# Kernel optimization log

Hardware: AMD Instinct MI355X
Metric: run time of the kernel (lower is better)

## Reference

```python
import jax, jax.numpy as jnp
import numpy as np

B, T, C = 2, 2048, 1024
N_HEAD = 16
HEAD_DIM = C // N_HEAD


def setup_inputs() -> dict:
    key = jax.random.key(0)
    k1, k2, k3, k4, k5 = jax.random.split(key, 5)
    s = 1.0 / np.sqrt(C)
    return {
        "x": jax.random.normal(k1, (B, T, C), dtype=jnp.float32),
        "w_attn": jax.random.normal(k2, (C, 3 * C), dtype=jnp.float32) * s,
        "b_attn": jax.random.normal(k3, (3 * C,), dtype=jnp.float32) * 0.02,
        "w_proj": jax.random.normal(k4, (C, C), dtype=jnp.float32) * s,
        "b_proj": jax.random.normal(k5, (C,), dtype=jnp.float32) * 0.02,
    }


def reference(x, w_attn, b_attn, w_proj, b_proj):
    Bx, Tx, Cx = x.shape
    qkv = x @ w_attn + b_attn  # [B, T, 3C]
    q, k, v = jnp.split(qkv, 3, axis=2)
    # [B, H, T, D]
    q = q.reshape(Bx, Tx, N_HEAD, HEAD_DIM).transpose(0, 2, 1, 3)
    k = k.reshape(Bx, Tx, N_HEAD, HEAD_DIM).transpose(0, 2, 1, 3)
    v = v.reshape(Bx, Tx, N_HEAD, HEAD_DIM).transpose(0, 2, 1, 3)
    scale = 1.0 / jnp.sqrt(jnp.asarray(HEAD_DIM, dtype=x.dtype))
    att = jnp.einsum("bhqd,bhkd->bhqk", q, k) * scale  # [B,H,T,T]
    causal = jnp.tril(jnp.ones((Tx, Tx), dtype=bool))
    att = jnp.where(causal[None, None, :, :], att, -jnp.inf)
    att = jax.nn.softmax(att, axis=-1)
    y = jnp.einsum("bhqk,bhkd->bhqd", att, v)  # [B,H,T,D]
    y = y.transpose(0, 2, 1, 3).reshape(Bx, Tx, Cx)
    return y @ w_proj + b_proj
```

## Files before the change

### kernel.cpp

```cpp
#include <hip/hip_runtime.h>
#include <hip/hip_bf16.h>
#include <stdint.h>

#define TT 2048
#define CC 1024
#define NH 16
#define HD 64
#define BT 4096

typedef float f32x4 __attribute__((ext_vector_type(4)));
typedef __bf16 bf16x8 __attribute__((ext_vector_type(8)));
typedef __bf16 bf16x4 __attribute__((ext_vector_type(4)));
typedef short sh4 __attribute__((ext_vector_type(4)));

#define MFMA(a, b, c) __builtin_amdgcn_mfma_f32_16x16x32_bf16((a), (b), (c), 0, 0, 0)
#define MFMA16(a, b, c) __builtin_amdgcn_mfma_f32_16x16x16bf16_1k((a), (b), (c), 0, 0, 0)

__device__ __forceinline__ void gload16(const void* g, void* l) {
    __builtin_amdgcn_global_load_lds(
        (const __attribute__((address_space(1))) void*)g,
        (__attribute__((address_space(3))) void*)l,
        16, 0, 0);
}

__global__ __launch_bounds__(256) void conv_f32_bf16(
    const float* __restrict__ in, __bf16* __restrict__ out, int n4) {
    int i = blockIdx.x * blockDim.x + threadIdx.x;
    int stride = gridDim.x * blockDim.x;
    for (; i < n4; i += stride) {
        float4 v = reinterpret_cast<const float4*>(in)[i];
        bf16x4 o;
        o.x = (__bf16)v.x; o.y = (__bf16)v.y; o.z = (__bf16)v.z; o.w = (__bf16)v.w;
        reinterpret_cast<bf16x4*>(out)[i] = o;
    }
}

__global__ __launch_bounds__(256) void transpose2_f32_bf16(
    const float* __restrict__ wa, __bf16* __restrict__ oa,
    const float* __restrict__ wp, __bf16* __restrict__ op) {
    __shared__ float tile[32][33];
    int bx = blockIdx.x;
    const float* in;
    __bf16* out;
    int C;
    if (bx < 96) { in = wa; out = oa; C = 3072; }
    else         { in = wp; out = op; C = 1024; bx -= 96; }
    int c0 = bx * 32, r0 = blockIdx.y * 32;
    int tx = threadIdx.x & 31, ty = (threadIdx.x >> 5) & 7;
#pragma unroll
    for (int j = 0; j < 32; j += 8)
        tile[ty + j][tx] = in[(size_t)(r0 + ty + j) * C + c0 + tx];
    __syncthreads();
#pragma unroll
    for (int j = 0; j < 32; j += 8)
        out[(size_t)(c0 + ty + j) * 1024 + r0 + tx] = (__bf16)tile[tx][ty + j];
}

template <int MODE>
__global__ __launch_bounds__(256) void gemm128(
    const __bf16* __restrict__ A, const __bf16* __restrict__ Bt,
    const float* __restrict__ bias,
    __bf16* __restrict__ oq, __bf16* __restrict__ ok, __bf16* __restrict__ ov,
    float* __restrict__ of, int M, int N, int K) {
    __shared__ __align__(16) __bf16 As[128 * 64];
    __shared__ __align__(16) __bf16 Bs[128 * 64];
    const int tid = threadIdx.x;
    const int w = tid >> 6, lane = tid & 63;
    const int l15 = lane & 15, lg = lane >> 4;
    const int m0 = blockIdx.y * 128, n0 = blockIdx.x * 128;
    const int wr = w >> 1, wc = w & 1;

    const f32x4 zero4 = {0.f, 0.f, 0.f, 0.f};
    f32x4 acc[4][4];
#pragma unroll
    for (int m = 0; m < 4; ++m)
#pragma unroll
        for (int n = 0; n < 4; ++n) acc[m][n] = zero4;

    const char* Ab = (const char*)A;
    const char* Bb = (const char*)Bt;
    const size_t rowbytes = (size_t)K * 2;

    for (int kt = 0; kt < K; kt += 64) {
#pragma unroll
        for (int j = 0; j < 4; ++j) {
            int base = (w * 4 + j) * 1024;
            int d0 = base + lane * 16;
            int row = d0 >> 7;
            int colb = d0 & 127;
            int scolb = colb ^ ((row & 7) << 4);
            gload16(Ab + (size_t)(m0 + row) * rowbytes + (size_t)kt * 2 + scolb,
                    (char*)As + base);
            gload16(Bb + (size_t)(n0 + row) * rowbytes + (size_t)kt * 2 + scolb,
                    (char*)Bs + base);
        }
        __syncthreads();
#pragma unroll
        for (int kk = 0; kk < 2; ++kk) {
            bf16x8 af[4], bfr[4];
#pragma unroll
            for (int m = 0; m < 4; ++m) {
                int row = wr * 64 + m * 16 + l15;
                int colb = kk * 64 + lg * 16;
                af[m] = *(const bf16x8*)((const char*)As + row * 128 +
                                         (colb ^ ((row & 7) << 4)));
            }
#pragma unroll
            for (int n = 0; n < 4; ++n) {
                int row = wc * 64 + n * 16 + l15;
                int colb = kk * 64 + lg * 16;
                bfr[n] = *(const bf16x8*)((const char*)Bs + row * 128 +
                                          (colb ^ ((row & 7) << 4)));
            }
#pragma unroll
            for (int m = 0; m < 4; ++m)
#pragma unroll
                for (int n = 0; n < 4; ++n)
                    acc[m][n] = MFMA(af[m], bfr[n], acc[m][n]);
        }
        __syncthreads();
    }

#pragma unroll
    for (int n = 0; n < 4; ++n) {
        int col = n0 + wc * 64 + n * 16 + l15;
        float bs = bias[col];
        if constexpr (MODE == 0) {
            int sec = col >> 10;
            int cc = col & 1023;
            int h = cc >> 6, d = cc & 63;
            if (sec == 2) {
#pragma unroll
                for (int m = 0; m < 4; ++m) {
                    int rowb = m0 + wr * 64 + m * 16 + lg * 4;
                    int bb = rowb >> 11, t = rowb & 2047;
                    bf16x4 pk;
#pragma unroll
                    for (int r = 0; r < 4; ++r) pk[r] = (__bf16)(acc[m][n][r] + bs);
                    *(bf16x4*)&ov[((size_t)(bb * NH + h) * HD + d) * TT + t] = pk;
                }
            } else {
                __bf16* dst = (sec == 0) ? oq : ok;
                float mult = (sec == 0) ? 0.125f * 1.44269504088896340736f : 1.0f;
#pragma unroll
                for (int m = 0; m < 4; ++m) {
                    int rowb = m0 + wr * 64 + m * 16 + lg * 4;
#pragma unroll
                    for (int r = 0; r < 4; ++r) {
                        int row = rowb + r;
                        int bb = row >> 11, t = row & 2047;
                        float val = (acc[m][n][r] + bs) * mult;
                        dst[((size_t)(bb * NH + h) * TT + t) * HD + d] = (__bf16)val;
                    }
                }
            }
        } else {
#pragma unroll
            for (int m = 0; m < 4; ++m) {
                int rowb = m0 + wr * 64 + m * 16 + lg * 4;
#pragma unroll
                for (int r = 0; r < 4; ++r) {
                    int row = rowb + r;
                    of[(size_t)row * N + col] = acc[m][n][r] + bs;
                }
            }
        }
    }
}

__global__ __launch_bounds__(256) void attn_kernel(
    const __bf16* __restrict__ q, const __bf16* __restrict__ k,
    const __bf16* __restrict__ vt, __bf16* __restrict__ y) {
    __shared__ __align__(16) __bf16 Kb[2][64 * 64];
    __shared__ __align__(16) __bf16 Vb[2][64 * 64];

    const int n = blockIdx.x;
    const int qt = 31 - (n >> 5);
    const int bh = ((n & 7) << 2) | ((n >> 3) & 3);
    const int tid = threadIdx.x, w = tid >> 6, lane = tid & 63;
    const int l15 = lane & 15, lg = lane >> 4;
    const char* kh = (const char*)(k + (size_t)bh * TT * HD);
    const char* vh = (const char*)(vt + (size_t)bh * HD * TT);
    const __bf16* qh = q + (size_t)bh * TT * HD;
    const int qbw = qt * 64 + w * 16;

    const f32x4 zero4 = {0.f, 0.f, 0.f, 0.f};
    float mrun = -1e30f, lrun = 0.f;
    f32x4 oacc[4];
    bf16x8 qf[2];
#pragma unroll
    for (int f = 0; f < 4; ++f) oacc[f] = zero4;
#pragma unroll
    for (int kk = 0; kk < 2; ++kk)
        qf[kk] = *(const bf16x8*)&qh[(size_t)(qbw + l15) * HD + kk * 32 + lg * 8];

    auto stage = [&](int kvb, int buf) {
#pragma unroll
        for (int j = 0; j < 2; ++j) {
            int d0 = ((w * 2 + j) * 64 + lane) * 16;
            int row = d0 >> 7, colb = d0 & 127;
            int scolb = colb ^ ((row & 7) << 4);
            gload16(kh + (size_t)(kvb + row) * 128 + scolb, (char*)Kb[buf] + d0);
            gload16(vh + (size_t)row * (TT * 2) + (size_t)kvb * 2 + scolb,
                    (char*)Vb[buf] + d0);
        }
    };

    stage(0, 0);
    __syncthreads();

    for (int g = 0; g <= qt; ++g) {
        const int cur = g & 1;
        if (g < qt) stage((g + 1) * 64, cur ^ 1);
        const int kb = g * 64;

        f32x4 s[4];
#pragma unroll
        for (int kf = 0; kf < 4; ++kf) s[kf] = zero4;
        __builtin_amdgcn_s_setprio(1);
#pragma unroll
        for (int kf = 0; kf < 4; ++kf) {
            int krow = kf * 16 + l15;
            const char* kr = (const char*)Kb[cur] + krow * 128;
            bf16x8 k0 = *(const bf16x8*)(kr + ((lg * 16) ^ ((krow & 7) << 4)));
            bf16x8 k1 = *(const bf16x8*)(kr + ((64 + lg * 16) ^ ((krow & 7) << 4)));
            s[kf] = MFMA(k0, qf[0], s[kf]);
            s[kf] = MFMA(k1, qf[1], s[kf]);
        }
        __builtin_amdgcn_s_setprio(0);
        if (g == qt) {
            const int qq = qbw + l15;
#pragma unroll
            for (int kf = 0; kf < 4; ++kf)
#pragma unroll
                for (int r = 0; r < 4; ++r) {
                    int kk_ = kb + kf * 16 + lg * 4 + r;
                    if (kk_ > qq) s[kf][r] = -1e30f;
                }
        }
        f32x4 m01, m23;
#pragma unroll
        for (int r = 0; r < 4; ++r) {
            m01[r] = fmaxf(s[0][r], s[1][r]);
            m23[r] = fmaxf(s[2][r], s[3][r]);
        }
        float m_ = fmaxf(fmaxf(fmaxf(m01[0], m01[1]), fmaxf(m01[2], m01[3])),
                         fmaxf(fmaxf(m23[0], m23[1]), fmaxf(m23[2], m23[3])));
        m_ = fmaxf(m_, __shfl_xor(m_, 16));
        m_ = fmaxf(m_, __shfl_xor(m_, 32));
        if (!__all(m_ <= mrun)) {
            float mn = fmaxf(mrun, m_);
            float fac = exp2f(mrun - mn);
            mrun = mn;
            lrun *= fac;
#pragma unroll
            for (int f = 0; f < 4; ++f)
#pragma unroll
                for (int r = 0; r < 4; ++r) oacc[f][r] *= fac;
        }
        float ss = 0.f;
        sh4 pb[4];
#pragma unroll
        for (int kf = 0; kf < 4; ++kf) {
            bf16x4 pk;
#pragma unroll
            for (int r = 0; r < 4; ++r) {
                float p = exp2f(s[kf][r] - mrun);
                pk[r] = (__bf16)p;
                ss += p;
            }
            pb[kf] = __builtin_bit_cast(sh4, pk);
        }
        lrun += ss;
        __builtin_amdgcn_s_setprio(1);
#pragma unroll
        for (int kf = 0; kf < 4; ++kf) {
#pragma unroll
            for (int f = 0; f < 4; ++f) {
                int vrow = f * 16 + l15;
                bf16x4 va = *(const bf16x4*)((const char*)Vb[cur] + vrow * 128 +
                                ((kf * 32 + lg * 8) ^ ((vrow & 7) << 4)));
                oacc[f] = MFMA16(__builtin_bit_cast(sh4, va), pb[kf], oacc[f]);
            }
        }
        __builtin_amdgcn_s_setprio(0);
        __syncthreads();
    }

    lrun += __shfl_xor(lrun, 16);
    lrun += __shfl_xor(lrun, 32);
    const int b = bh >> 4, h = bh & 15;
    float inv = 1.0f / lrun;
#pragma unroll
    for (int f = 0; f < 4; ++f) {
        bf16x4 pk;
#pragma unroll
        for (int r = 0; r < 4; ++r) pk[r] = (__bf16)(oacc[f][r] * inv);
        *(bf16x4*)&y[(size_t)(b * TT + qbw + l15) * CC + h * 64 + f * 16 +
                     lg * 4] = pk;
    }
}

extern "C" void kernel_launch(void* const* d_in, const int* in_sizes, int n_in,
                              void* d_out, int out_size, void* d_ws, size_t ws_size,
                              hipStream_t stream) {
    const float* x      = (const float*)d_in[0];
    const float* w_attn = (const float*)d_in[1];
    const float* b_attn = (const float*)d_in[2];
    const float* w_proj = (const float*)d_in[3];
    const float* b_proj = (const float*)d_in[4];
    float* out = (float*)d_out;

    char* ws = (char*)d_ws;
    size_t off = 0;
    auto alloc = [&](size_t bytes) {
        char* p = ws + off;
        off += (bytes + 255) & ~(size_t)255;
        return p;
    };
    __bf16* xb   = (__bf16*)alloc((size_t)BT * CC * 2);
    __bf16* watb = (__bf16*)alloc((size_t)3 * CC * CC * 2);
    __bf16* wptb = (__bf16*)alloc((size_t)CC * CC * 2);
    __bf16* qb   = (__bf16*)alloc((size_t)BT * CC * 2);
    __bf16* kbuf = (__bf16*)alloc((size_t)BT * CC * 2);
    __bf16* vtb  = (__bf16*)alloc((size_t)BT * CC * 2);
    __bf16* yb   = (__bf16*)alloc((size_t)BT * CC * 2);

    conv_f32_bf16<<<1024, 256, 0, stream>>>(x, xb, BT * CC / 4);
    transpose2_f32_bf16<<<dim3(128, 32), 256, 0, stream>>>(
        w_attn, watb, w_proj, wptb);

    gemm128<0><<<dim3(3 * CC / 128, BT / 128), 256, 0, stream>>>(
        xb, watb, b_attn, qb, kbuf, vtb, nullptr, BT, 3 * CC, CC);

    attn_kernel<<<1024, 256, 0, stream>>>(qb, kbuf, vtb, yb);

    gemm128<1><<<dim3(CC / 128, BT / 128), 256, 0, stream>>>(
        yb, wptb, b_proj, nullptr, nullptr, nullptr, out, BT, CC, CC);
}
```

Baseline: 118.2 us.

## Widen attention KV tile to 128 keys and pre-swizzle V in the QKV epilogue

The attention loop now processes 128 keys per iteration instead of 64. That halves the number of loop trips and barriers and doubles the MFMA work between synchronisations. The QKV GEMM epilogue writes transposed V with an XOR swizzle baked into its global layout, so the attention kernel can copy contiguous 256-byte rows into LDS and read them conflict-free. In exchange, LDS use per block doubles, which may lower occupancy. On diagonal tiles where the query tile index is even, half of the last 128-key tile is fully masked and computed for nothing.

```diff
diff --git a/kernel.cpp b/kernel.cpp
--- a/kernel.cpp
+++ b/kernel.cpp
@@ -137,7 +137,10 @@
                     bf16x4 pk;
 #pragma unroll
                     for (int r = 0; r < 4; ++r) pk[r] = (__bf16)(acc[m][n][r] + bs);
-                    *(bf16x4*)&ov[((size_t)(bb * NH + h) * HD + d) * TT + t] = pk;
+                    size_t base = ((size_t)(bb * NH + h) * HD + d) * (TT * 2);
+                    size_t byte = base + (size_t)((t & ~63) * 2 +
+                                   (((t & 63) * 2) ^ ((d & 15) << 3)));
+                    *(bf16x4*)((char*)ov + byte) = pk;
                 }
             } else {
                 __bf16* dst = (sec == 0) ? oq : ok;
@@ -171,8 +174,8 @@
 __global__ __launch_bounds__(256) void attn_kernel(
     const __bf16* __restrict__ q, const __bf16* __restrict__ k,
     const __bf16* __restrict__ vt, __bf16* __restrict__ y) {
-    __shared__ __align__(16) __bf16 Kb[2][64 * 64];
-    __shared__ __align__(16) __bf16 Vb[2][64 * 64];
+    __shared__ __align__(16) __bf16 Kb[2][128 * 64];
+    __shared__ __align__(16) __bf16 Vb[2][64 * 128];
 
     const int n = blockIdx.x;
     const int qt = 31 - (n >> 5);
@@ -183,6 +186,7 @@
     const char* vh = (const char*)(vt + (size_t)bh * HD * TT);
     const __bf16* qh = q + (size_t)bh * TT * HD;
     const int qbw = qt * 64 + w * 16;
+    const int nt = (qt >> 1) + 1;
 
     const f32x4 zero4 = {0.f, 0.f, 0.f, 0.f};
     float mrun = -1e30f, lrun = 0.f;
@@ -196,30 +200,36 @@
 
     auto stage = [&](int kvb, int buf) {
 #pragma unroll
-        for (int j = 0; j < 2; ++j) {
-            int d0 = ((w * 2 + j) * 64 + lane) * 16;
-            int row = d0 >> 7, colb = d0 & 127;
-            int scolb = colb ^ ((row & 7) << 4);
-            gload16(kh + (size_t)(kvb + row) * 128 + scolb, (char*)Kb[buf] + d0);
-            gload16(vh + (size_t)row * (TT * 2) + (size_t)kvb * 2 + scolb,
-                    (char*)Vb[buf] + d0);
+        for (int j = 0; j < 4; ++j) {
+            int d0 = ((w * 4 + j) * 64 + lane) * 16;
+            {
+                int row = d0 >> 7, colb = d0 & 127;
+                int scolb = colb ^ ((row & 7) << 4);
+                gload16(kh + (size_t)(kvb + row) * 128 + scolb,
+                        (char*)Kb[buf] + d0);
+            }
+            {
+                int row = d0 >> 8, colb = d0 & 255;
+                gload16(vh + (size_t)row * (TT * 2) + (size_t)kvb * 2 + colb,
+                        (char*)Vb[buf] + d0);
+            }
         }
     };
 
     stage(0, 0);
     __syncthreads();
 
-    for (int g = 0; g <= qt; ++g) {
+    for (int g = 0; g < nt; ++g) {
         const int cur = g & 1;
-        if (g < qt) stage((g + 1) * 64, cur ^ 1);
-        const int kb = g * 64;
-
-        f32x4 s[4];
-#pragma unroll
-        for (int kf = 0; kf < 4; ++kf) s[kf] = zero4;
+        if (g + 1 < nt) stage((g + 1) * 128, cur ^ 1);
+        const int kb = g * 128;
+
+        f32x4 s[8];
+#pragma unroll
+        for (int kf = 0; kf < 8; ++kf) s[kf] = zero4;
         __builtin_amdgcn_s_setprio(1);
 #pragma unroll
-        for (int kf = 0; kf < 4; ++kf) {
+        for (int kf = 0; kf < 8; ++kf) {
             int krow = kf * 16 + l15;
             const char* kr = (const char*)Kb[cur] + krow * 128;
             bf16x8 k0 = *(const bf16x8*)(kr + ((lg * 16) ^ ((krow & 7) << 4)));
@@ -228,24 +238,27 @@
             s[kf] = MFMA(k1, qf[1], s[kf]);
         }
         __builtin_amdgcn_s_setprio(0);
-        if (g == qt) {
+        if (g == nt - 1) {
             const int qq = qbw + l15;
 #pragma unroll
-            for (int kf = 0; kf < 4; ++kf)
+            for (int kf = 0; kf < 8; ++kf)
 #pragma unroll
                 for (int r = 0; r < 4; ++r) {
                     int kk_ = kb + kf * 16 + lg * 4 + r;
                     if (kk_ > qq) s[kf][r] = -1e30f;
                 }
         }
-        f32x4 m01, m23;
-#pragma unroll
-        for (int r = 0; r < 4; ++r) {
-            m01[r] = fmaxf(s[0][r], s[1][r]);
-            m23[r] = fmaxf(s[2][r], s[3][r]);
-        }
-        float m_ = fmaxf(fmaxf(fmaxf(m01[0], m01[1]), fmaxf(m01[2], m01[3])),
-                         fmaxf(fmaxf(m23[0], m23[1]), fmaxf(m23[2], m23[3])));
+        f32x4 mv0 = s[0], mv1 = s[1];
+#pragma unroll
+        for (int kf = 2; kf < 8; kf += 2) {
+#pragma unroll
+            for (int r = 0; r < 4; ++r) {
+                mv0[r] = fmaxf(mv0[r], s[kf][r]);
+                mv1[r] = fmaxf(mv1[r], s[kf + 1][r]);
+            }
+        }
+        float m_ = fmaxf(fmaxf(fmaxf(mv0[0], mv0[1]), fmaxf(mv0[2], mv0[3])),
+                         fmaxf(fmaxf(mv1[0], mv1[1]), fmaxf(mv1[2], mv1[3])));
         m_ = fmaxf(m_, __shfl_xor(m_, 16));
         m_ = fmaxf(m_, __shfl_xor(m_, 32));
         if (!__all(m_ <= mrun)) {
@@ -259,9 +272,9 @@
                 for (int r = 0; r < 4; ++r) oacc[f][r] *= fac;
         }
         float ss = 0.f;
-        sh4 pb[4];
-#pragma unroll
-        for (int kf = 0; kf < 4; ++kf) {
+        sh4 pb[8];
+#pragma unroll
+        for (int kf = 0; kf < 8; ++kf) {
             bf16x4 pk;
 #pragma unroll
             for (int r = 0; r < 4; ++r) {
@@ -274,12 +287,13 @@
         lrun += ss;
         __builtin_amdgcn_s_setprio(1);
 #pragma unroll
-        for (int kf = 0; kf < 4; ++kf) {
+        for (int kf = 0; kf < 8; ++kf) {
+            int blk = (kf >= 4) ? 128 : 0;
+            int cb = (((kf & 3) * 32 + lg * 8) ^ (l15 << 3)) + blk;
 #pragma unroll
             for (int f = 0; f < 4; ++f) {
                 int vrow = f * 16 + l15;
-                bf16x4 va = *(const bf16x4*)((const char*)Vb[cur] + vrow * 128 +
-                                ((kf * 32 + lg * 8) ^ ((vrow & 7) << 4)));
+                bf16x4 va = *(const bf16x4*)((const char*)Vb[cur] + vrow * 256 + cb);
                 oacc[f] = MFMA16(__builtin_bit_cast(sh4, va), pb[kf], oacc[f]);
             }
         }
```

New measurement: 121.8 us. +3.1%, slower.
